# Kernel tuning notes

Measured on AMD Instinct MI355X. Metric: run time of the kernel, lower is better.

The kernel has to match this reference:

```python
import jax, jax.numpy as jnp
import numpy as np

K = 9        # kernel_size
DIL = 6      # dilation
SIGMA = 1.0  # gaussian bandwidth
BN_EPS = 1e-5


def setup_inputs() -> dict:
    key = jax.random.key(0)
    ks = jax.random.split(key, 6)
    B, Cin, Cout, N = 8, 256, 256, 8192
    x = jax.random.normal(ks[0], (B, Cin, N), jnp.float32)
    coords = jax.random.normal(ks[1], (B, 3, N), jnp.float32)
    rotations = jax.random.normal(ks[2], (B, 3, N), jnp.float32)
    distances = jax.random.uniform(ks[3], (B, N), jnp.float32)
    W = jax.random.normal(ks[4], (Cout, Cin, K), jnp.float32) * 0.02
    bias = jnp.zeros((Cout,), jnp.float32)
    gamma = jnp.ones((Cout,), jnp.float32)
    beta = jnp.zeros((Cout,), jnp.float32)
    return dict(x=x, coords=coords, rotations=rotations, distances=distances,
                W=W, bias=bias, gamma=gamma, beta=beta)


def _tap_weight(c0, cj, r0, rj, d0, dj, sigma):
    # Gaussian weight from 3D coordinate offset + curve-distance offset,
    # modulated by rotation alignment |cos(r_i, r_j)|.
    dc = jnp.sum((c0 - cj) ** 2, axis=1)          # [B,N]
    dd = (d0 - dj) ** 2                            # [B,N]
    g = jnp.exp(-(dc + dd) / (2.0 * sigma * sigma))
    num = jnp.sum(r0 * rj, axis=1)
    den = jnp.sqrt(jnp.sum(r0 * r0, axis=1) * jnp.sum(rj * rj, axis=1)) + 1e-8
    return g * jnp.abs(num / den)                  # [B,N]


def reference(x, coords, rotations, distances, W, bias, gamma, beta):
    B, Cin, N = x.shape
    Cout = W.shape[0]
    pad = DIL * (K // 2)  # same-length output for the dilated conv
    pw3 = ((0, 0), (0, 0), (pad, pad))
    xp = jnp.pad(x, pw3)
    cp = jnp.pad(coords, pw3)
    rp = jnp.pad(rotations, pw3)
    dp = jnp.pad(distances, ((0, 0), (pad, pad)))

    out = jnp.zeros((B, Cout, N), x.dtype)
    for k in range(K):  # fixed, small tap loop
        off = k * DIL
        xk = jax.lax.dynamic_slice_in_dim(xp, off, N, axis=2)
        ck = jax.lax.dynamic_slice_in_dim(cp, off, N, axis=2)
        rk = jax.lax.dynamic_slice_in_dim(rp, off, N, axis=2)
        dk = jax.lax.dynamic_slice_in_dim(dp, off, N, axis=1)
        g = _tap_weight(coords, ck, rotations, rk, distances, dk, SIGMA)  # [B,N]
        out = out + jnp.einsum('oc,bcn->bon', W[:, :, k], xk * g[:, None, :])
    out = out + bias[None, :, None]

    # BatchNorm1d (training-mode batch stats over B and N per channel)
    mean = jnp.mean(out, axis=(0, 2), keepdims=True)
    var = jnp.var(out, axis=(0, 2), keepdims=True)
    out = (out - mean) / jnp.sqrt(var + BN_EPS)
    out = out * gamma[None, :, None] + beta[None, :, None]
    return jax.nn.relu(out)
```

## Files before the change

### kernel.cpp

```cpp
#include <hip/hip_runtime.h>

#define KTAPS 9
#define DIL 6
#define BN_EPS 1e-5f
#define BB 8
#define CIN 256
#define COUT 256
#define NPTS 8192
#define BN 64
#define XOFF 32
#define BSTRIDE 40

typedef __attribute__((ext_vector_type(8))) short short8;
typedef __attribute__((ext_vector_type(4))) float f32x4;

__device__ __forceinline__ unsigned short f2bf(float f) {
  union { float f; unsigned u; } v; v.f = f;
  unsigned r = v.u + 0x7fffu + ((v.u >> 16) & 1u);
  return (unsigned short)(r >> 16);
}

__device__ __forceinline__ void async16(const void* gp, void* lp) {
  __builtin_amdgcn_global_load_lds(
      (const __attribute__((address_space(1))) unsigned int*)gp,
      (__attribute__((address_space(3))) unsigned int*)lp, 16, 0, 0);
}

__global__ __launch_bounds__(256)
void pre_kernel(const float* __restrict__ W, short* __restrict__ Wa,
                float* __restrict__ sums) {
  int bid = blockIdx.x;
  if (bid < 2304) {
    int idx = bid * 256 + threadIdx.x;
    int kk = idx & 31;
    int mi = (idx >> 5) & 255;
    int chunk = idx >> 13;
    int ktap = chunk >> 3;
    int c = ((chunk & 7) << 5) + kk;
    Wa[idx] = (short)f2bf(W[(size_t)mi * (CIN * KTAPS) + c * KTAPS + ktap]);
  } else {
    if (threadIdx.x < 512) sums[threadIdx.x] = 0.f;
  }
}

__global__ __launch_bounds__(256, 3)
void conv_mfma(const float* __restrict__ x, const float* __restrict__ coords,
               const float* __restrict__ rot, const float* __restrict__ dist,
               const short* __restrict__ Wa, const float* __restrict__ bias,
               float* __restrict__ out,
               float* __restrict__ sums1, float* __restrict__ sums2) {
  __shared__ float x_win[2][4][32][32];
  __shared__ short B_lds[2][BN][BSTRIDE];
  __shared__ float g_lds[KTAPS][BN];

  const int tid = threadIdx.x;
  const int b = blockIdx.y;
  const int n0 = blockIdx.x * BN;
  const int wave = tid >> 6;
  const int lane = tid & 63;
  const int col = lane & 15;
  const int quad = lane >> 4;

  {
    const float* cb = coords + (size_t)b * 3 * NPTS;
    const float* rb = rot + (size_t)b * 3 * NPTS;
    const float* db = dist + (size_t)b * NPTS;
    const int n = n0 + lane;
    float c0x = cb[n], c0y = cb[NPTS + n], c0z = cb[2 * NPTS + n];
    float r0x = rb[n], r0y = rb[NPTS + n], r0z = rb[2 * NPTS + n];
    float d0 = db[n];
    float r0n = r0x * r0x + r0y * r0y + r0z * r0z;
    for (int k = wave; k < KTAPS; k += 4) {
      int j = n + (k - KTAPS / 2) * DIL;
      float gv = 0.f;
      if (j >= 0 && j < NPTS) {
        float dcx = c0x - cb[j], dcy = c0y - cb[NPTS + j], dcz = c0z - cb[2 * NPTS + j];
        float dc = dcx * dcx + dcy * dcy + dcz * dcz;
        float dd = d0 - db[j];
        dd *= dd;
        float gauss = expf(-(dc + dd) * 0.5f);
        float rjx = rb[j], rjy = rb[NPTS + j], rjz = rb[2 * NPTS + j];
        float num = r0x * rjx + r0y * rjy + r0z * rjz;
        float den = sqrtf(r0n * (rjx * rjx + rjy * rjy + rjz * rjz)) + 1e-8f;
        gv = gauss * fabsf(num / den);
      }
      g_lds[k][lane] = gv;
    }
  }

  const float* xb = x + (size_t)b * CIN * NPTS;
  const int arow0 = (wave * 64 + col) * 32 + quad * 8;
  const int wrB = lane * BSTRIDE + ((wave ^ ((lane >> 3) & 3)) << 3);

  short8 af[2][4];

#define LOADAF(AF, CHUNK)                                               \
  {                                                                     \
    const short* p_ = Wa + (size_t)(CHUNK) * 8192 + arow0;              \
    _Pragma("unroll")                                                   \
    for (int m = 0; m < 4; ++m) AF[m] = *(const short8*)(p_ + m * 512); \
  }

#define STAGE_DMA(C8N)                                                  \
  {                                                                     \
    const int buf_ = (C8N)&1;                                           \
    const int ch_ = wave * 8 + (lane >> 3);                             \
    const float* gr_ = xb + (size_t)((C8N)*32 + ch_) * NPTS;            \
    const int cg_ = (lane & 7) * 4;                                     \
    _Pragma("unroll")                                                   \
    for (int q_ = 0; q_ < 4; ++q_) {                                    \
      int jg_ = n0 - XOFF + q_ * 32 + cg_;                              \
      jg_ = jg_ < 0 ? 0 : (jg_ > NPTS - 4 ? NPTS - 4 : jg_);            \
      async16(gr_ + jg_, (float*)&x_win[buf_][q_][wave * 8][0] + lane * 4); \
    }                                                                   \
  }

#define BUILD(K, P, XC)                                                 \
  {                                                                     \
    float g_ = g_lds[K][lane];                                          \
    const int w_ = lane + ((K)-KTAPS / 2) * DIL + XOFF;                 \
    const float* xp_ = &x_win[XC][0][0][0] + ((w_ >> 5) << 10) + (w_ & 31) + wave * 256; \
    short8 p_;                                                          \
    _Pragma("unroll")                                                   \
    for (int cc = 0; cc < 8; ++cc)                                      \
      p_[cc] = (short)f2bf(xp_[cc * 32] * g_);                          \
    *(short8*)(&B_lds[P][0][0] + wrB) = p_;                             \
  }

#define MFMA_TAP(P, AF)                                                 \
  {                                                                     \
    const short* bb_ = &B_lds[P][0][0];                                 \
    _Pragma("unroll")                                                   \
    for (int j = 0; j < 4; ++j) {                                       \
      short8 bfv_ = *(const short8*)(bb_ + (j * 16 + col) * BSTRIDE +   \
                                     ((quad ^ ((2 * j + (col >> 3)) & 3)) << 3)); \
      _Pragma("unroll")                                                 \
      for (int m = 0; m < 4; ++m)                                       \
        acc[m][j] = __builtin_amdgcn_mfma_f32_16x16x32_bf16(AF[m], bfv_, acc[m][j], 0, 0, 0); \
    }                                                                   \
  }

#define BAR()                                                           \
  {                                                                     \
    asm volatile("s_waitcnt lgkmcnt(0)" ::: "memory");                  \
    __builtin_amdgcn_s_barrier();                                       \
    __builtin_amdgcn_sched_barrier(0);                                  \
  }

#define BARFULL()                                                       \
  {                                                                     \
    asm volatile("s_waitcnt vmcnt(0) lgkmcnt(0)" ::: "memory");         \
    __builtin_amdgcn_s_barrier();                                       \
    __builtin_amdgcn_sched_barrier(0);                                  \
  }

#define TAPX(K, C8)                                                     \
  {                                                                     \
    LOADAF(af[((K) + 1 + ((C8)&1)) & 1], 8 * ((K) + 1) + (C8));         \
    BUILD((K) + 1, ((C8) + (K) + 1) & 1, (C8)&1);                       \
    MFMA_TAP(((C8) + (K)) & 1, af[((K) + ((C8)&1)) & 1]);               \
    BAR();                                                              \
  }

#define C8BODY(C8, DN)                                                  \
  {                                                                     \
    if (DN) STAGE_DMA((C8) + 1);                                        \
    TAPX(0, C8)                                                         \
    TAPX(1, C8)                                                         \
    TAPX(2, C8)                                                         \
    TAPX(3, C8)                                                         \
    TAPX(4, C8)                                                         \
    TAPX(5, C8)                                                         \
    TAPX(6, C8)                                                         \
    TAPX(7, C8)                                                         \
          \
    BARFULL();                                                          \
    if (DN) {                                                           \
      LOADAF(af[((C8) + 1) & 1], (C8) + 1);                             \
      BUILD(0, ((C8) + 1) & 1, ((C8) + 1) & 1);                         \
    }                                                                   \
    MFMA_TAP((C8)&1, af[(C8)&1]);                                       \
    BAR();                                                              \
  }

  f32x4 acc[4][4];
#pragma unroll
  for (int m = 0; m < 4; ++m)
#pragma unroll
    for (int j = 0; j < 4; ++j) acc[m][j] = (f32x4)0.f;

  STAGE_DMA(0);
  LOADAF(af[0], 0);
  asm volatile("s_waitcnt vmcnt(0)" ::: "memory");
  __syncthreads();
  BUILD(0, 0, 0);
  __syncthreads();

#pragma unroll 1
  for (int c2 = 0; c2 < 4; ++c2) {
    const int c8a = 2 * c2;
    const int c8b = 2 * c2 + 1;
    const bool dnb = (c2 < 3);
    C8BODY(c8a, true);
    C8BODY(c8b, dnb);
  }

  const int obase = wave * 64;
  float* outp = out + (size_t)b * COUT * NPTS + n0;
#pragma unroll
  for (int m = 0; m < 4; ++m) {
    const int o0 = obase + m * 16 + quad * 4;
    const float4 bv = *(const float4*)&bias[o0];
#pragma unroll
    for (int j = 0; j < 4; ++j) {
      acc[m][j][0] += bv.x; acc[m][j][1] += bv.y;
      acc[m][j][2] += bv.z; acc[m][j][3] += bv.w;
    }
#pragma unroll
    for (int r = 0; r < 4; ++r) {
      float s1 = 0.f, s2 = 0.f;
#pragma unroll
      for (int j = 0; j < 4; ++j) {
        float v = acc[m][j][r];
        s1 += v; s2 += v * v;
      }
      s1 += __shfl_xor(s1, 1); s2 += __shfl_xor(s2, 1);
      s1 += __shfl_xor(s1, 2); s2 += __shfl_xor(s2, 2);
      s1 += __shfl_xor(s1, 4); s2 += __shfl_xor(s2, 4);
      s1 += __shfl_xor(s1, 8); s2 += __shfl_xor(s2, 8);
      if (col == 0) {
        atomicAdd(&sums1[o0 + r], s1);
        atomicAdd(&sums2[o0 + r], s2);
      }
#pragma unroll
      for (int j = 0; j < 4; ++j)
        outp[(size_t)(o0 + r) * NPTS + j * 16 + col] = acc[m][j][r];
    }
  }
}

__global__ __launch_bounds__(256)
void bn_apply(float* __restrict__ out, const float* __restrict__ sums1,
              const float* __restrict__ sums2, const float* __restrict__ gamma,
              const float* __restrict__ beta) {
  int bo = blockIdx.x;
  int o = bo & (COUT - 1);
  const float inv = 1.f / (float)(BB * NPTS);
  float mean = sums1[o] * inv;
  float var = sums2[o] * inv - mean * mean;
  float scale = gamma[o] * rsqrtf(var + BN_EPS);
  float shift = beta[o] - mean * scale;
  float4* p = (float4*)(out + (size_t)bo * NPTS);
  for (int i = threadIdx.x; i < NPTS / 4; i += blockDim.x) {
    float4 v = p[i];
    v.x = fmaxf(fmaf(v.x, scale, shift), 0.f);
    v.y = fmaxf(fmaf(v.y, scale, shift), 0.f);
    v.z = fmaxf(fmaf(v.z, scale, shift), 0.f);
    v.w = fmaxf(fmaf(v.w, scale, shift), 0.f);
    p[i] = v;
  }
}

extern "C" void kernel_launch(void* const* d_in, const int* in_sizes, int n_in,
                              void* d_out, int out_size, void* d_ws, size_t ws_size,
                              hipStream_t stream) {
  const float* x      = (const float*)d_in[0];
  const float* coords = (const float*)d_in[1];
  const float* rot    = (const float*)d_in[2];
  const float* dist   = (const float*)d_in[3];
  const float* W      = (const float*)d_in[4];
  const float* bias   = (const float*)d_in[5];
  const float* gamma  = (const float*)d_in[6];
  const float* beta   = (const float*)d_in[7];
  float* out = (float*)d_out;

  float* ws    = (float*)d_ws;
  float* sums1 = ws;
  float* sums2 = ws + 256;
  short* Wa    = (short*)(ws + 512);

  pre_kernel<<<2305, 256, 0, stream>>>(W, Wa, sums1);
  conv_mfma<<<dim3(NPTS / BN, BB), 256, 0, stream>>>(x, coords, rot, dist, Wa, bias, out, sums1, sums2);
  bn_apply<<<BB * COUT, 256, 0, stream>>>(out, sums1, sums2, gamma, beta);
}
```

Before: 313.0 us.

## Batch three taps per barrier stage with triple-tap LDS buffers

Restructures the conv main loop so each pipeline stage builds and consumes three taps at once, using a [2][3] ping-pong set of B tiles in LDS and three A-fragment register sets. This cuts the block barriers per input-channel chunk from nine to three and gives the scheduler more independent MFMA and LDS work between syncs. In exchange, LDS use and register pressure rise, and launch bounds drop from 3 to 2 blocks per CU, which lowers occupancy.

New measurement: 309.7 us. No clear change (-1.1%).

```diff
diff --git a/kernel.cpp b/kernel.cpp
--- a/kernel.cpp
+++ b/kernel.cpp
@@ -43,14 +43,14 @@
   }
 }
 
-__global__ __launch_bounds__(256, 3)
+__global__ __launch_bounds__(256, 2)
 void conv_mfma(const float* __restrict__ x, const float* __restrict__ coords,
                const float* __restrict__ rot, const float* __restrict__ dist,
                const short* __restrict__ Wa, const float* __restrict__ bias,
                float* __restrict__ out,
                float* __restrict__ sums1, float* __restrict__ sums2) {
   __shared__ float x_win[2][4][32][32];
-  __shared__ short B_lds[2][BN][BSTRIDE];
+  __shared__ short Bt[2][3][BN][BSTRIDE];
   __shared__ float g_lds[KTAPS][BN];
 
   const int tid = threadIdx.x;
@@ -92,7 +92,7 @@
   const int arow0 = (wave * 64 + col) * 32 + quad * 8;
   const int wrB = lane * BSTRIDE + ((wave ^ ((lane >> 3) & 3)) << 3);
 
-  short8 af[2][4];
+  short8 af0[4], af1[4], af2[4];
 
 #define LOADAF(AF, CHUNK)                                               \
   {                                                                     \
@@ -115,7 +115,7 @@
     }                                                                   \
   }
 
-#define BUILD(K, P, XC)                                                 \
+#define BUILDT(K, S, PP, XC)                                            \
   {                                                                     \
     float g_ = g_lds[K][lane];                                          \
     const int w_ = lane + ((K)-KTAPS / 2) * DIL + XOFF;                 \
@@ -124,12 +124,12 @@
     _Pragma("unroll")                                                   \
     for (int cc = 0; cc < 8; ++cc)                                      \
       p_[cc] = (short)f2bf(xp_[cc * 32] * g_);                          \
-    *(short8*)(&B_lds[P][0][0] + wrB) = p_;                             \
-  }
-
-#define MFMA_TAP(P, AF)                                                 \
-  {                                                                     \
-    const short* bb_ = &B_lds[P][0][0];                                 \
+    *(short8*)(&Bt[PP][S][0][0] + wrB) = p_;                            \
+  }
+
+#define MFMAT(S, PP, AF)                                                \
+  {                                                                     \
+    const short* bb_ = &Bt[PP][S][0][0];                                \
     _Pragma("unroll")                                                   \
     for (int j = 0; j < 4; ++j) {                                       \
       short8 bfv_ = *(const short8*)(bb_ + (j * 16 + col) * BSTRIDE +   \
@@ -154,33 +154,38 @@
     __builtin_amdgcn_sched_barrier(0);                                  \
   }
 
-#define TAPX(K, C8)                                                     \
-  {                                                                     \
-    LOADAF(af[((K) + 1 + ((C8)&1)) & 1], 8 * ((K) + 1) + (C8));         \
-    BUILD((K) + 1, ((C8) + (K) + 1) & 1, (C8)&1);                       \
-    MFMA_TAP(((C8) + (K)) & 1, af[((K) + ((C8)&1)) & 1]);               \
+#define REGION01(C8, R, P, DN)                                          \
+  {                                                                     \
+    LOADAF(af0, (3 * (R) + 0) * 8 + (C8));                              \
+    LOADAF(af1, (3 * (R) + 1) * 8 + (C8));                              \
+    LOADAF(af2, (3 * (R) + 2) * 8 + (C8));                              \
+    if (DN) STAGE_DMA((C8) + 1);                                        \
+    BUILDT(3 * (R) + 3, 0, (P) ^ 1, (C8)&1);                            \
+    BUILDT(3 * (R) + 4, 1, (P) ^ 1, (C8)&1);                            \
+    BUILDT(3 * (R) + 5, 2, (P) ^ 1, (C8)&1);                            \
+    MFMAT(0, (P), af0);                                                 \
+    MFMAT(1, (P), af1);                                                 \
+    MFMAT(2, (P), af2);                                                 \
     BAR();                                                              \
   }
 
-#define C8BODY(C8, DN)                                                  \
-  {                                                                     \
-    if (DN) STAGE_DMA((C8) + 1);                                        \
-    TAPX(0, C8)                                                         \
-    TAPX(1, C8)                                                         \
-    TAPX(2, C8)                                                         \
-    TAPX(3, C8)                                                         \
-    TAPX(4, C8)                                                         \
-    TAPX(5, C8)                                                         \
-    TAPX(6, C8)                                                         \
-    TAPX(7, C8)                                                         \
-          \
-    BARFULL();                                                          \
+#define REGION2(C8, P, DN)                                              \
+  {                                                                     \
+    LOADAF(af0, 48 + (C8));                                             \
+    LOADAF(af1, 56 + (C8));                                             \
+    LOADAF(af2, 64 + (C8));                                             \
+    MFMAT(0, (P), af0);                                                 \
+    MFMAT(1, (P), af1);                                                 \
     if (DN) {                                                           \
-      LOADAF(af[((C8) + 1) & 1], (C8) + 1);                             \
-      BUILD(0, ((C8) + 1) & 1, ((C8) + 1) & 1);                         \
+      BARFULL();                                                        \
+      BUILDT(0, 0, (P) ^ 1, ((C8) + 1) & 1);                            \
+      BUILDT(1, 1, (P) ^ 1, ((C8) + 1) & 1);                            \
+      BUILDT(2, 2, (P) ^ 1, ((C8) + 1) & 1);                            \
+      MFMAT(2, (P), af2);                                               \
+      BAR();                                                            \
+    } else {                                                            \
+      MFMAT(2, (P), af2);                                               \
     }                                                                   \
-    MFMA_TAP((C8)&1, af[(C8)&1]);                                       \
-    BAR();                                                              \
   }
 
   f32x4 acc[4][4];
@@ -190,19 +195,20 @@
     for (int j = 0; j < 4; ++j) acc[m][j] = (f32x4)0.f;
 
   STAGE_DMA(0);
-  LOADAF(af[0], 0);
   asm volatile("s_waitcnt vmcnt(0)" ::: "memory");
   __syncthreads();
-  BUILD(0, 0, 0);
+  BUILDT(0, 0, 0, 0);
+  BUILDT(1, 1, 0, 0);
+  BUILDT(2, 2, 0, 0);
   __syncthreads();
 
 #pragma unroll 1
-  for (int c2 = 0; c2 < 4; ++c2) {
-    const int c8a = 2 * c2;
-    const int c8b = 2 * c2 + 1;
-    const bool dnb = (c2 < 3);
-    C8BODY(c8a, true);
-    C8BODY(c8b, dnb);
+  for (int c8 = 0; c8 < 8; ++c8) {
+    const int P0 = c8 & 1;
+    const bool dn = (c8 < 7);
+    REGION01(c8, 0, P0, dn);
+    REGION01(c8, 1, P0 ^ 1, false);
+    REGION2(c8, P0, dn);
   }
 
   const int obase = wave * 64;
```
